# Performance work log

Hardware: AMD Instinct MI355X
Metric: run time of the kernel (lower is better)

## Reference

```python
import jax, jax.numpy as jnp
import numpy as np

B, T, C, K = 256, 336, 512, 3
CLAMP_LO, CLAMP_HI = 1e-4, 1.0 - 1e-4


def setup_inputs() -> dict:
    key = jax.random.key(0)
    k1, k2 = jax.random.split(key)
    x = jax.random.normal(k1, (B, T, C), dtype=jnp.float32)
    # learned params: logit_alpha [K, C], mix_logits [C, K]
    # initialize logit_alpha near logit(init_alphas) with small noise so sigmoid(.) stays ~[0.75, 0.99]
    init_alphas = jnp.array([0.8, 0.9, 0.98], dtype=jnp.float32)
    base = jnp.log(init_alphas / (1.0 - init_alphas))  # logit
    logit_alpha = base[:, None] + 0.05 * jax.random.normal(k2, (K, C), dtype=jnp.float32)
    mix_logits = jnp.zeros((C, K), dtype=jnp.float32)
    return {"x": x, "logit_alpha": logit_alpha, "mix_logits": mix_logits}


def reference(x, logit_alpha, mix_logits):
    Bx, Tx, Cx = x.shape
    a = jnp.clip(jax.nn.sigmoid(logit_alpha), CLAMP_LO, CLAMP_HI).astype(x.dtype)  # [K, C]
    t_idx = jnp.arange(Tx, dtype=x.dtype)[:, None, None]                          # [T, 1, 1]
    a_pow = a[None, :, :] ** t_idx                                                # [T, K, C]
    # weights: a^t, multiplied by (1 - a) for t >= 1
    scale = jnp.where(t_idx > 0, 1.0 - a[None, :, :], jnp.ones_like(a)[None])     # [T, K, C]
    weights = a_pow * scale                                                       # [T, K, C]
    divisor = jnp.maximum(a_pow, 1e-8)                                            # [T, K, C]
    xw = x[:, :, None, :] * weights[None]                                         # [B, T, K, C]
    yk = jnp.cumsum(xw, axis=1) / divisor[None]                                   # [B, T, K, C]
    mix = jax.nn.softmax(mix_logits.astype(x.dtype), axis=-1).T                   # [K, C]
    trend = jnp.sum(yk * mix[None, None, :, :], axis=2)                           # [B, T, C]
    return trend
```

## Files before the change

kernel.cpp:

```cpp
#include <hip/hip_runtime.h>

namespace {
constexpr int kB     = 256;
constexpr int kT     = 336;
constexpr int kC     = 512;
constexpr int kK     = 3;
constexpr int kU     = 16;
constexpr int kWaves = 4;
}

#define WAITV(n) do { asm volatile("s_waitcnt vmcnt(" #n ")" ::: "memory"); \
                      __builtin_amdgcn_sched_barrier(0); } while (0)

__global__ __launch_bounds__(256) void ema_mix_kernel(
    const float* __restrict__ x,
    const float* __restrict__ logit_alpha,
    const float* __restrict__ mix_logits,
    float* __restrict__ out)
{
    __shared__ float bufA[kWaves][kU][64];
    __shared__ float bufB[kWaves][kU][64];

    const int lane = threadIdx.x & 63;
    const int w    = threadIdx.x >> 6;
    const int c    = ((blockIdx.x & 1) << 8) | (w << 6) | lane;
    const int b    = blockIdx.x >> 1;

    float a[kK], oma[kK], inva[kK], mixw[kK];
    {
        float logits[kK];
        float lmax = -3.402823e38f;
        #pragma unroll
        for (int k = 0; k < kK; ++k) {
            logits[k] = mix_logits[c * kK + k];
            lmax = fmaxf(lmax, logits[k]);
        }
        float esum = 0.f;
        #pragma unroll
        for (int k = 0; k < kK; ++k) {
            logits[k] = expf(logits[k] - lmax);
            esum += logits[k];
        }
        const float rs = 1.0f / esum;
        #pragma unroll
        for (int k = 0; k < kK; ++k) {
            mixw[k] = logits[k] * rs;
            const float z = logit_alpha[k * kC + c];
            float s;
            if (z >= 0.f) {
                s = 1.0f / (1.0f + expf(-z));
            } else {
                const float e = expf(z);
                s = e / (1.0f + e);
            }
            s = fminf(fmaxf(s, 1e-4f), (float)(1.0 - 1e-4));
            a[k]    = s;
            oma[k]  = 1.0f - s;
            inva[k] = 1.0f / s;
        }
    }

    asm volatile("s_waitcnt vmcnt(0)" ::: "memory");
    __builtin_amdgcn_sched_barrier(0);

    const float* xp = x   + (size_t)b * (kT * kC) + c;
    float*       op = out + (size_t)b * (kT * kC) + c;

    float apow[kK], vinv[kK], S[kK];
    #pragma unroll
    for (int k = 0; k < kK; ++k) { apow[k] = 1.f; vinv[k] = 1.f; S[k] = 0.f; }

    auto stage = [&](float (&buf)[kWaves][kU][64], int ch) {
        const float* g = xp + (size_t)ch * (kU * kC);
        #pragma unroll
        for (int r = 0; r < kU; ++r) {
            __builtin_amdgcn_global_load_lds(
                (const __attribute__((address_space(1))) void*)(g + (size_t)r * kC),
                (__attribute__((address_space(3))) void*)(&buf[w][r][0]),
                4, 0, 0);
        }
    };

    auto compute = [&](float (&buf)[kWaves][kU][64], int ch, bool first) {
        const int tbase = ch * kU;
        #pragma unroll
        for (int i = 0; i < kU; ++i) {
            const float xv = buf[w][i][lane];
            float o = 0.f;
            #pragma unroll
            for (int k = 0; k < kK; ++k) {
                const float wt = (first && i == 0) ? 1.0f : apow[k] * oma[k];
                S[k] = fmaf(xv, wt, S[k]);
                o = fmaf(S[k] * mixw[k], fminf(vinv[k], 1e8f), o);
                apow[k] *= a[k];
                vinv[k] *= inva[k];
            }
            __builtin_nontemporal_store(o, &op[(size_t)(tbase + i) * kC]);
        }
    };

    stage(bufA, 0);
    stage(bufB, 1);  WAITV(16);  compute(bufA, 0, true);
    #pragma unroll 1
    for (int kk = 1; kk <= 17; kk += 2) {
        stage(bufA, kk + 1);  WAITV(32);  compute(bufB, kk,     false);
        stage(bufB, kk + 2);  WAITV(32);  compute(bufA, kk + 1, false);
    }
    stage(bufA, 20);  WAITV(32);  compute(bufB, 19, false);
    WAITV(16);  compute(bufA, 20, false);
}

extern "C" void kernel_launch(void* const* d_in, const int* in_sizes, int n_in,
                              void* d_out, int out_size, void* d_ws, size_t ws_size,
                              hipStream_t stream) {
    const float* x  = (const float*)d_in[0];
    const float* la = (const float*)d_in[1];
    const float* ml = (const float*)d_in[2];
    float* o = (float*)d_out;

    const int blocks = kB * (kC / 256);
    ema_mix_kernel<<<dim3(blocks), dim3(256), 0, stream>>>(x, la, ml, o);
}
```

Measured before the change: 58.36 us.

## Deepen async prefetch to 8-buffer ring with 16-byte global-to-LDS loads

Replaces the 16-row double buffer with an 8-slot ring of 8-row chunks, keeping six chunks of loads in flight ahead of compute. The per-row 4-byte global_load_lds calls become two 16-byte loads per chunk. Each lane now fetches four contiguous floats, and the LDS layout is kept row-major so the compute reads stay unchanged. The aim is more memory-level parallelism and fewer load instructions. In exchange, LDS per block doubles to 64KB, which can limit how many blocks fit on a CU, and the hand-tuned vmcnt counts now have to account for interleaved stores.

```diff
diff --git a/kernel.cpp b/kernel.cpp
--- a/kernel.cpp
+++ b/kernel.cpp
@@ -5,7 +5,9 @@
 constexpr int kT     = 336;
 constexpr int kC     = 512;
 constexpr int kK     = 3;
-constexpr int kU     = 16;
+constexpr int kR     = 8;
+constexpr int kNCH   = kT / kR;
+constexpr int kNB    = 8;
 constexpr int kWaves = 4;
 }
 
@@ -18,12 +20,12 @@
     const float* __restrict__ mix_logits,
     float* __restrict__ out)
 {
-    __shared__ float bufA[kWaves][kU][64];
-    __shared__ float bufB[kWaves][kU][64];
+    __shared__ float buf[kNB][kWaves][kR][64];
 
     const int lane = threadIdx.x & 63;
     const int w    = threadIdx.x >> 6;
-    const int c    = ((blockIdx.x & 1) << 8) | (w << 6) | lane;
+    const int c0w  = ((blockIdx.x & 1) << 8) | (w << 6);
+    const int c    = c0w | lane;
     const int b    = blockIdx.x >> 1;
 
     float a[kK], oma[kK], inva[kK], mixw[kK];
@@ -63,29 +65,32 @@
     asm volatile("s_waitcnt vmcnt(0)" ::: "memory");
     __builtin_amdgcn_sched_barrier(0);
 
-    const float* xp = x   + (size_t)b * (kT * kC) + c;
-    float*       op = out + (size_t)b * (kT * kC) + c;
+    const float* xbase = x + (size_t)b * (kT * kC);
+    float*       op    = out + (size_t)b * (kT * kC) + c;
+
+    const int roff = lane >> 4;
+    const int scol = c0w + ((lane & 15) << 2);
 
     float apow[kK], vinv[kK], S[kK];
     #pragma unroll
     for (int k = 0; k < kK; ++k) { apow[k] = 1.f; vinv[k] = 1.f; S[k] = 0.f; }
 
-    auto stage = [&](float (&buf)[kWaves][kU][64], int ch) {
-        const float* g = xp + (size_t)ch * (kU * kC);
+    auto stage = [&](int ch, int bi) {
         #pragma unroll
-        for (int r = 0; r < kU; ++r) {
+        for (int q = 0; q < 2; ++q) {
+            const float* g = xbase + ((size_t)(ch * kR + q * 4 + roff) * kC + scol);
             __builtin_amdgcn_global_load_lds(
-                (const __attribute__((address_space(1))) void*)(g + (size_t)r * kC),
-                (__attribute__((address_space(3))) void*)(&buf[w][r][0]),
-                4, 0, 0);
+                (const __attribute__((address_space(1))) void*)g,
+                (__attribute__((address_space(3))) void*)(&buf[bi][w][q * 4][0]),
+                16, 0, 0);
         }
     };
 
-    auto compute = [&](float (&buf)[kWaves][kU][64], int ch, bool first) {
-        const int tbase = ch * kU;
+    auto compute = [&](int ch, int bi, bool first) {
+        const int tbase = ch * kR;
         #pragma unroll
-        for (int i = 0; i < kU; ++i) {
-            const float xv = buf[w][i][lane];
+        for (int i = 0; i < kR; ++i) {
+            const float xv = buf[bi][w][i][lane];
             float o = 0.f;
             #pragma unroll
             for (int k = 0; k < kK; ++k) {
@@ -99,15 +104,29 @@
         }
     };
 
-    stage(bufA, 0);
-    stage(bufB, 1);  WAITV(16);  compute(bufA, 0, true);
+    stage(0, 0); stage(1, 1); stage(2, 2);
+    stage(3, 3); stage(4, 4); stage(5, 5);
+
+    WAITV(10); stage( 6, 6); compute(0, 0, true);
+    WAITV(18); stage( 7, 7); compute(1, 1, false);
+    WAITV(26); stage( 8, 0); compute(2, 2, false);
+    WAITV(34); stage( 9, 1); compute(3, 3, false);
+    WAITV(42); stage(10, 2); compute(4, 4, false);
+    WAITV(50); stage(11, 3); compute(5, 5, false);
+
     #pragma unroll 1
-    for (int kk = 1; kk <= 17; kk += 2) {
-        stage(bufA, kk + 1);  WAITV(32);  compute(bufB, kk,     false);
-        stage(bufB, kk + 2);  WAITV(32);  compute(bufA, kk + 1, false);
+    for (int k = 6; k <= 35; ++k) {
+        WAITV(58);
+        stage(k + 6, (k + 6) & 7);
+        compute(k, k & 7, false);
     }
-    stage(bufA, 20);  WAITV(32);  compute(bufB, 19, false);
-    WAITV(16);  compute(bufA, 20, false);
+
+    WAITV(58); compute(36, 36 & 7, false);
+    WAITV(56); compute(37, 37 & 7, false);
+    WAITV(54); compute(38, 38 & 7, false);
+    WAITV(52); compute(39, 39 & 7, false);
+    WAITV(50); compute(40, 40 & 7, false);
+    WAITV(48); compute(41, 41 & 7, false);
 }
 
 extern "C" void kernel_launch(void* const* d_in, const int* in_sizes, int n_in,
```

Measured after the change: 57.85 us. About the same (-0.9%).
